# Optimization experiments

Hardware: AMD Instinct MI355X
Metric: run time of the kernel (lower is better)

## Reference

```python
import jax, jax.numpy as jnp
import numpy as np

VOCAB = 32000
D_MODEL = 768
N_LAYERS = 2
D_STATE = 16
D_CONV = 4
EXPAND = 2
D_INNER = EXPAND * D_MODEL            # 1536
DT_RANK = (D_MODEL + 15) // 16        # 48
B, L = 2, 1024


def setup_inputs() -> dict:
    key = jax.random.key(0)
    ks = jax.random.split(key, 10)
    n = lambda k, shape, s=0.02: jax.random.normal(k, shape, jnp.float32) * s
    A_log = jnp.broadcast_to(
        jnp.log(jnp.arange(1, D_STATE + 1, dtype=jnp.float32)),
        (N_LAYERS, D_INNER, D_STATE)).copy()
    return {
        "x": jax.random.randint(ks[0], (B, L), 0, VOCAB, jnp.int32),
        "embedding": n(ks[1], (VOCAB, D_MODEL)),
        "in_proj_w": n(ks[2], (N_LAYERS, 2 * D_INNER, D_MODEL)),
        "conv_w": n(ks[3], (N_LAYERS, D_INNER, D_CONV), 0.1),
        "conv_b": jnp.zeros((N_LAYERS, D_INNER), jnp.float32),
        "x_proj_w": n(ks[4], (N_LAYERS, DT_RANK + 2 * D_STATE, D_INNER)),
        "dt_proj_w": n(ks[5], (N_LAYERS, D_INNER, DT_RANK), 0.1),
        "dt_proj_b": jnp.full((N_LAYERS, D_INNER), -4.6, jnp.float32),  # softplus(-4.6)~0.01
        "A_log": A_log,
        "D_param": jnp.ones((N_LAYERS, D_INNER), jnp.float32),
        "out_proj_w": n(ks[6], (N_LAYERS, D_MODEL, D_INNER)),
        "ln_w": jnp.ones((D_MODEL,), jnp.float32),
        "ln_b": jnp.zeros((D_MODEL,), jnp.float32),
    }


def _causal_conv1d(x, w, b):
    # x: (B,L,Din), w: (Din,K) depthwise, b: (Din,)  -> (B,L,Din), causal
    Din, K = w.shape
    xt = jnp.transpose(x, (0, 2, 1))  # (B,Din,L)
    out = jax.lax.conv_general_dilated(
        xt, w[:, None, :], window_strides=(1,), padding=[(K - 1, 0)],
        feature_group_count=Din)
    return jnp.transpose(out, (0, 2, 1)) + b


def _selective_scan(u, dt, A, Bm, Cm, Dp):
    # u,dt: (B,L,Din); A: (Din,N); Bm,Cm: (B,L,N); Dp: (Din,)
    dA = jnp.exp(jnp.einsum('bld,dn->bldn', dt, A))          # (B,L,Din,N)
    dBu = jnp.einsum('bld,bln,bld->bldn', dt, Bm, u)          # (B,L,Din,N)

    def step(h, inp):
        dA_t, dBu_t, C_t = inp
        h = dA_t * h + dBu_t                                   # (B,Din,N)
        y = jnp.einsum('bdn,bn->bd', h, C_t)
        return h, y

    h0 = jnp.zeros((u.shape[0], u.shape[2], A.shape[1]), u.dtype)
    _, ys = jax.lax.scan(step, h0, (dA.transpose(1, 0, 2, 3),
                                    dBu.transpose(1, 0, 2, 3),
                                    Cm.transpose(1, 0, 2)))
    return ys.transpose(1, 0, 2) + u * Dp                      # (B,L,Din)


def _mamba_block(h, in_w, cw, cb, xp_w, dt_w, dt_b, A_log, Dp, out_w):
    xz = jnp.einsum('bld,ed->ble', h, in_w)                    # (B,L,2*Din)
    x_in, z = jnp.split(xz, 2, axis=-1)
    xc = jax.nn.silu(_causal_conv1d(x_in, cw, cb))             # (B,L,Din)
    x_dbl = jnp.einsum('bld,ed->ble', xc, xp_w)                # (B,L,dt_rank+2N)
    dt, Bm, Cm = jnp.split(x_dbl, [DT_RANK, DT_RANK + D_STATE], axis=-1)
    dt = jax.nn.softplus(jnp.einsum('blr,dr->bld', dt, dt_w) + dt_b)
    A = -jnp.exp(A_log)                                        # (Din,N)
    y = _selective_scan(xc, dt, A, Bm, Cm, Dp)
    y = y * jax.nn.silu(z)
    return jnp.einsum('bld,ed->ble', y, out_w)                 # (B,L,d_model)


def _layer_norm(x, w, b, eps=1e-5):
    mu = x.mean(-1, keepdims=True)
    var = ((x - mu) ** 2).mean(-1, keepdims=True)
    return (x - mu) * jax.lax.rsqrt(var + eps) * w + b


def reference(x, embedding, in_proj_w, conv_w, conv_b, x_proj_w, dt_proj_w,
              dt_proj_b, A_log, D_param, out_proj_w, ln_w, ln_b):
    h = embedding[x]                                           # (B,L,d_model)
    for i in range(N_LAYERS):
        h = _mamba_block(h, in_proj_w[i], conv_w[i], conv_b[i], x_proj_w[i],
                         dt_proj_w[i], dt_proj_b[i], A_log[i], D_param[i],
                         out_proj_w[i]) + h
    h = _layer_norm(h, ln_w, ln_b)
    return jnp.einsum('bld,vd->blv', h, embedding)             # tied lm_head
```

## Files before the change

kernel.cpp:

```cpp
#include <hip/hip_runtime.h>
#include <hip/hip_bf16.h>

typedef __bf16 bf16_t;
typedef __bf16 bf16x8 __attribute__((ext_vector_type(8)));
typedef float floatx4 __attribute__((ext_vector_type(4)));

#define D_MODEL 768
#define D_INNER 1536
#define D_STATE 16
#define DT_RANK 48
#define NROWS 2048
#define LSEQ 1024
#define SCAN_C 32
#define SCAN_RPC 32
#define SCAN_NDG 24
#define SCAN_STRIDE 24576

__global__ void detect_kernel(const unsigned int* __restrict__ lnw, int* __restrict__ flag) {
  if (threadIdx.x == 0 && blockIdx.x == 0)
    *flag = (lnw[0] == 0x3F800000u) ? 0 : 1;
}

struct CvtSrcs { const void* p[11]; };

__global__ __launch_bounds__(256) void cvt_all(CvtSrcs sp, bf16_t* __restrict__ wk,
                                               int total, const int* __restrict__ flagp) {
  int i = blockIdx.x * 256 + threadIdx.x;
  if (i >= total) return;
  const int off[12] = {0, 4718592, 4730880, 4733952, 4979712, 5127168, 5130240,
                       5179392, 5182464, 7541760, 7542528, 7543296};
  const void* src = sp.p[0];
  int base = 0;
#pragma unroll
  for (int k = 1; k <= 10; k++) {
    if (i >= off[k]) { src = sp.p[k]; base = off[k]; }
  }
  int j = i - base;
  float v = (*flagp) ? (float)((const bf16_t*)src)[j] : ((const float*)src)[j];
  wk[i] = (bf16_t)v;
}

__global__ __launch_bounds__(256) void cvt_emb(const void* __restrict__ src,
                                               bf16_t* __restrict__ dst,
                                               const int* __restrict__ flagp) {
  int i = blockIdx.x * 256 + threadIdx.x;
  const int nchunk = 32000 * 768 / 8;
  if (i >= nchunk) return;
  if (*flagp) {
    ((uint4*)dst)[i] = ((const uint4*)src)[i];
  } else {
    const float4* s = (const float4*)src + (size_t)i * 2;
    float4 f0 = s[0], f1 = s[1];
    bf16x8 v;
    v[0] = (bf16_t)f0.x; v[1] = (bf16_t)f0.y; v[2] = (bf16_t)f0.z; v[3] = (bf16_t)f0.w;
    v[4] = (bf16_t)f1.x; v[5] = (bf16_t)f1.y; v[6] = (bf16_t)f1.z; v[7] = (bf16_t)f1.w;
    *(bf16x8*)(dst + (size_t)i * 8) = v;
  }
}

__global__ __launch_bounds__(256) void embed_kernel(const int* __restrict__ x,
                                                    const void* __restrict__ emb,
                                                    float* __restrict__ h,
                                                    bf16_t* __restrict__ hb,
                                                    const int* __restrict__ flagp) {
  int isbf = *flagp;
  int idx = blockIdx.x * 256 + threadIdx.x;
  if (idx >= NROWS * D_MODEL) return;
  int row = idx / D_MODEL, c = idx - row * D_MODEL;
  size_t o = (size_t)x[row] * D_MODEL + c;
  float v = isbf ? (float)((const bf16_t*)emb)[o] : ((const float*)emb)[o];
  h[idx] = v;
  hb[idx] = (bf16_t)v;
}

typedef __attribute__((address_space(3))) void lds_void_t;
typedef __attribute__((address_space(1))) void glb_void_t;

__device__ __forceinline__ void gload16(const void* g, void* l) {
  __builtin_amdgcn_global_load_lds((const glb_void_t*)(unsigned long long)g,
                                   (lds_void_t*)(unsigned long long)l, 16, 0, 0);
}

__global__ __launch_bounds__(256) void gemm_bt(const bf16_t* __restrict__ A,
                                               const void* __restrict__ Bw,
                                               int M, int N, int K, int mode,
                                               float* __restrict__ Cf,
                                               bf16_t* __restrict__ Cb,
                                               const float* __restrict__ res,
                                               const int* __restrict__ flagp,
                                               int swapgrid) {
  __shared__ __align__(16) bf16_t As[128 * 64];
  __shared__ __align__(16) bf16_t Bs[128 * 64];
  int bNative = flagp ? (*flagp == 0) : 0;
  int tid = threadIdx.x;
  int nb = swapgrid ? blockIdx.y : blockIdx.x;
  int mb = swapgrid ? blockIdx.x : blockIdx.y;
  int m0 = mb * 128, n0 = nb * 128;
  int wave = tid >> 6, lane = tid & 63;
  int wr = wave >> 1, wc = wave & 1;
  int m16 = lane & 15, ksel = lane >> 4;
  int srow = lane >> 3;
  int sseg = lane & 7;

  floatx4 acc[4][4];
#pragma unroll
  for (int i = 0; i < 4; i++)
#pragma unroll
    for (int j = 0; j < 4; j++) acc[i][j] = (floatx4){0.f, 0.f, 0.f, 0.f};

  for (int k0 = 0; k0 < K; k0 += 64) {
#pragma unroll
    for (int i = 0; i < 4; i++) {
      int j = wave * 4 + i;
      int row = j * 8 + srow;
      int sg = sseg ^ (row & 7);
      gload16(A + (size_t)(m0 + row) * K + k0 + sg * 8, &As[j * 512]);
    }
    if (!bNative) {
#pragma unroll
      for (int i = 0; i < 4; i++) {
        int j = wave * 4 + i;
        int row = j * 8 + srow;
        int sg = sseg ^ (row & 7);
        gload16((const bf16_t*)Bw + (size_t)(n0 + row) * K + k0 + sg * 8, &Bs[j * 512]);
      }
    } else {
#pragma unroll
      for (int rep = 0; rep < 4; rep++) {
        int l = tid + rep * 256;
        int row = l >> 3, sg = l & 7;
        const float* gb = (const float*)Bw + (size_t)(n0 + row) * K + k0 + sg * 8;
        float4 f0 = *(const float4*)gb;
        float4 f1 = *(const float4*)(gb + 4);
        bf16x8 v;
        v[0] = (bf16_t)f0.x; v[1] = (bf16_t)f0.y; v[2] = (bf16_t)f0.z; v[3] = (bf16_t)f0.w;
        v[4] = (bf16_t)f1.x; v[5] = (bf16_t)f1.y; v[6] = (bf16_t)f1.z; v[7] = (bf16_t)f1.w;
        *(bf16x8*)&Bs[row * 64 + (sg ^ (row & 7)) * 8] = v;
      }
    }
    __syncthreads();
#pragma unroll
    for (int kk = 0; kk < 2; kk++) {
      int ck = (ksel + 4 * kk) ^ (lane & 7);
      bf16x8 aF[4], bF[4];
#pragma unroll
      for (int mi = 0; mi < 4; mi++)
        aF[mi] = *(const bf16x8*)&As[(wr * 64 + mi * 16 + m16) * 64 + ck * 8];
#pragma unroll
      for (int ni = 0; ni < 4; ni++)
        bF[ni] = *(const bf16x8*)&Bs[(wc * 64 + ni * 16 + m16) * 64 + ck * 8];
#pragma unroll
      for (int mi = 0; mi < 4; mi++)
#pragma unroll
        for (int ni = 0; ni < 4; ni++)
          acc[mi][ni] = __builtin_amdgcn_mfma_f32_16x16x32_bf16(aF[mi], bF[ni], acc[mi][ni], 0, 0, 0);
    }
    __syncthreads();
  }

#pragma unroll
  for (int mi = 0; mi < 4; mi++)
#pragma unroll
    for (int ni = 0; ni < 4; ni++)
#pragma unroll
      for (int r = 0; r < 4; r++) {
        int row = m0 + wr * 64 + mi * 16 + ksel * 4 + r;
        int col = n0 + wc * 64 + ni * 16 + m16;
        size_t off = (size_t)row * N + col;
        float v = acc[mi][ni][r];
        if (mode == 0) {
          Cf[off] = v;
        } else if (mode == 1) {
          float o = v + res[off];
          Cf[off] = o;
          Cb[off] = (bf16_t)o;
        } else {
          Cf[off] = v;
        }
      }
}

__global__ __launch_bounds__(256) void conv_silu(const float* __restrict__ xz,
                                                 const bf16_t* __restrict__ cw,
                                                 const bf16_t* __restrict__ cb,
                                                 bf16_t* __restrict__ xc) {
  int idx = blockIdx.x * 256 + threadIdx.x;
  if (idx >= NROWS * D_INNER) return;
  int d = idx % D_INNER;
  int row = idx / D_INNER;
  int l = row % LSEQ;
  int base = row - l;
  float s = (float)cb[d];
#pragma unroll
  for (int k = 0; k < 4; k++) {
    int ll = l - 3 + k;
    if (ll >= 0) s += (float)cw[d * 4 + k] * xz[(size_t)(base + ll) * (2 * D_INNER) + d];
  }
  float sil = s / (1.f + __expf(-s));
  xc[idx] = (bf16_t)sil;
}

__device__ inline float bflo(unsigned int u) { return __uint_as_float(u << 16); }
__device__ inline float bfhi(unsigned int u) { return __uint_as_float(u & 0xffff0000u); }

__global__ __launch_bounds__(128) void xproj_kernel(const bf16_t* __restrict__ xc,
                                                    const bf16_t* __restrict__ W,
                                                    float* __restrict__ xdbl) {
  __shared__ unsigned int srow[D_INNER / 2];
  int row = blockIdx.x;
  const unsigned int* src = (const unsigned int*)(xc + (size_t)row * D_INNER);
  for (int i = threadIdx.x; i < D_INNER / 2; i += 128) srow[i] = src[i];
  __syncthreads();
  int j = threadIdx.x;
  if (j < DT_RANK + 2 * D_STATE) {
    const unsigned int* wr = (const unsigned int*)(W + (size_t)j * D_INNER);
    float s = 0.f;
    for (int i = 0; i < D_INNER / 2; i++) {
      unsigned int a = srow[i], w = wr[i];
      s = fmaf(bflo(a), bflo(w), s);
      s = fmaf(bfhi(a), bfhi(w), s);
    }
    xdbl[(size_t)row * 80 + j] = s;
  }
}

__global__ __launch_bounds__(256) void dtproj_kernel(const float* __restrict__ xdbl,
                                                     const bf16_t* __restrict__ W,
                                                     const bf16_t* __restrict__ bias,
                                                     float* __restrict__ dt) {
  int idx = blockIdx.x * 256 + threadIdx.x;
  if (idx >= NROWS * D_INNER) return;
  int d = idx % D_INNER;
  int row = idx / D_INNER;
  const bf16_t* wr = W + (size_t)d * DT_RANK;
  const float* xr = xdbl + (size_t)row * 80;
  float s = (float)bias[d];
#pragma unroll 8
  for (int r = 0; r < DT_RANK; r++) s = fmaf(xr[r], (float)wr[r], s);
  float sp = (s > 20.f) ? s : log1pf(__expf(s));
  dt[idx] = sp;
}

__global__ __launch_bounds__(64) void scan_p1(const float* __restrict__ dt_,
                                              const bf16_t* __restrict__ xc,
                                              const float* __restrict__ xdbl,
                                              const bf16_t* __restrict__ A_log,
                                              float* __restrict__ P,
                                              float* __restrict__ F) {
  int wg = blockIdx.x;
  int dgrp = wg % SCAN_NDG, c2 = wg / SCAN_NDG;
  int b = c2 >> 5, c = c2 & 31;
  int d = dgrp * 64 + threadIdx.x;
  int r0 = b * LSEQ + c * SCAN_RPC;

  float Adn[16];
  {
    bf16x8 a0 = *(const bf16x8*)(A_log + (size_t)d * 16);
    bf16x8 a1 = *(const bf16x8*)(A_log + (size_t)d * 16 + 8);
#pragma unroll
    for (int n = 0; n < 8; n++) { Adn[n] = -__expf((float)a0[n]); Adn[n + 8] = -__expf((float)a1[n]); }
  }
  float h[16], p[16];
#pragma unroll
  for (int n = 0; n < 16; n++) { h[n] = 0.f; p[n] = 1.f; }

  float dtv = dt_[(size_t)r0 * D_INNER + d];
  float uv = (float)xc[(size_t)r0 * D_INNER + d];
  float Bv[16];
  {
    const float4* bp = (const float4*)(xdbl + (size_t)r0 * 80 + DT_RANK);
#pragma unroll
    for (int q = 0; q < 4; q++) *(float4*)&Bv[q * 4] = bp[q];
  }

  for (int i = 0; i < SCAN_RPC; i++) {
    int rn = r0 + i + 1;
    float dtn = dt_[(size_t)rn * D_INNER + d];
    float un = (float)xc[(size_t)rn * D_INNER + d];
    float Bn[16];
    {
      const float4* bp = (const float4*)(xdbl + (size_t)rn * 80 + DT_RANK);
#pragma unroll
      for (int q = 0; q < 4; q++) *(float4*)&Bn[q * 4] = bp[q];
    }
    float dtu = dtv * uv;
#pragma unroll
    for (int n = 0; n < 16; n++) {
      float dA = __expf(dtv * Adn[n]);
      h[n] = fmaf(dA, h[n], dtu * Bv[n]);
      p[n] *= dA;
    }
    dtv = dtn; uv = un;
#pragma unroll
    for (int n = 0; n < 16; n++) Bv[n] = Bn[n];
  }

  size_t o = (size_t)c2 * SCAN_STRIDE + (size_t)d * 16;
#pragma unroll
  for (int q = 0; q < 4; q++) {
    *(float4*)(P + o + q * 4) = *(float4*)&p[q * 4];
    *(float4*)(F + o + q * 4) = *(float4*)&h[q * 4];
  }
}

__global__ __launch_bounds__(256) void scan_p2(const float* __restrict__ P,
                                               const float* __restrict__ F,
                                               float* __restrict__ Hin) {
  int gid = blockIdx.x * 256 + threadIdx.x;
  if (gid >= 2 * SCAN_STRIDE) return;
  int b = gid / SCAN_STRIDE, j = gid - b * SCAN_STRIDE;
  float pP[SCAN_C], pF[SCAN_C];
#pragma unroll
  for (int c = 0; c < SCAN_C; c++) {
    size_t o = (size_t)(b * SCAN_C + c) * SCAN_STRIDE + j;
    pP[c] = P[o]; pF[c] = F[o];
  }
  float h = 0.f;
#pragma unroll
  for (int c = 0; c < SCAN_C; c++) {
    size_t o = (size_t)(b * SCAN_C + c) * SCAN_STRIDE + j;
    Hin[o] = h;
    h = fmaf(pP[c], h, pF[c]);
  }
}

__global__ __launch_bounds__(64) void scan_p3(const float* __restrict__ dt_,
                                              const bf16_t* __restrict__ xc,
                                              const float* __restrict__ xdbl,
                                              const float* __restrict__ xz,
                                              const bf16_t* __restrict__ A_log,
                                              const bf16_t* __restrict__ Dp,
                                              const float* __restrict__ Hin,
                                              bf16_t* __restrict__ yg) {
  int wg = blockIdx.x;
  int dgrp = wg % SCAN_NDG, c2 = wg / SCAN_NDG;
  int b = c2 >> 5, c = c2 & 31;
  int d = dgrp * 64 + threadIdx.x;
  int r0 = b * LSEQ + c * SCAN_RPC;

  float Adn[16];
  {
    bf16x8 a0 = *(const bf16x8*)(A_log + (size_t)d * 16);
    bf16x8 a1 = *(const bf16x8*)(A_log + (size_t)d * 16 + 8);
#pragma unroll
    for (int n = 0; n < 8; n++) { Adn[n] = -__expf((float)a0[n]); Adn[n + 8] = -__expf((float)a1[n]); }
  }
  float Dd = (float)Dp[d];
  float h[16];
  {
    size_t o = (size_t)c2 * SCAN_STRIDE + (size_t)d * 16;
#pragma unroll
    for (int q = 0; q < 4; q++) *(float4*)&h[q * 4] = *(const float4*)(Hin + o + q * 4);
  }

  float dtv = dt_[(size_t)r0 * D_INNER + d];
  float uv = (float)xc[(size_t)r0 * D_INNER + d];
  float zv = xz[(size_t)r0 * (2 * D_INNER) + D_INNER + d];
  float Bv[16], Cv[16];
  {
    const float4* bp = (const float4*)(xdbl + (size_t)r0 * 80 + DT_RANK);
#pragma unroll
    for (int q = 0; q < 4; q++) *(float4*)&Bv[q * 4] = bp[q];
#pragma unroll
    for (int q = 0; q < 4; q++) *(float4*)&Cv[q * 4] = bp[q + 4];
  }

  for (int i = 0; i < SCAN_RPC; i++) {
    int r = r0 + i;
    int rn = r + 1;
    float dtn = dt_[(size_t)rn * D_INNER + d];
    float un = (float)xc[(size_t)rn * D_INNER + d];
    float zn = xz[(size_t)rn * (2 * D_INNER) + D_INNER + d];
    float Bn[16], Cn[16];
    {
      const float4* bp = (const float4*)(xdbl + (size_t)rn * 80 + DT_RANK);
#pragma unroll
      for (int q = 0; q < 4; q++) *(float4*)&Bn[q * 4] = bp[q];
#pragma unroll
      for (int q = 0; q < 4; q++) *(float4*)&Cn[q * 4] = bp[q + 4];
    }
    float dtu = dtv * uv;
    float y = 0.f;
#pragma unroll
    for (int n = 0; n < 16; n++) {
      float dA = __expf(dtv * Adn[n]);
      h[n] = fmaf(dA, h[n], dtu * Bv[n]);
      y = fmaf(h[n], Cv[n], y);
    }
    float sil = zv / (1.f + __expf(-zv));
    yg[(size_t)r * D_INNER + d] = (bf16_t)((y + Dd * uv) * sil);
    dtv = dtn; uv = un; zv = zn;
#pragma unroll
    for (int n = 0; n < 16; n++) { Bv[n] = Bn[n]; Cv[n] = Cn[n]; }
  }
}

__global__ __launch_bounds__(256) void ln_kernel(const float* __restrict__ h,
                                                 const bf16_t* __restrict__ w,
                                                 const bf16_t* __restrict__ b,
                                                 bf16_t* __restrict__ out) {
  __shared__ float s1[4], s2[4];
  int row = blockIdx.x;
  int tid = threadIdx.x, lane = tid & 63, wave = tid >> 6;
  const float* hr = h + (size_t)row * D_MODEL;
  float a = 0.f, a2 = 0.f;
  for (int i = tid; i < D_MODEL; i += 256) {
    float v = hr[i];
    a += v; a2 += v * v;
  }
#pragma unroll
  for (int m = 32; m >= 1; m >>= 1) {
    a += __shfl_xor(a, m, 64);
    a2 += __shfl_xor(a2, m, 64);
  }
  if (lane == 0) { s1[wave] = a; s2[wave] = a2; }
  __syncthreads();
  float sum = s1[0] + s1[1] + s1[2] + s1[3];
  float sum2 = s2[0] + s2[1] + s2[2] + s2[3];
  float mu = sum / D_MODEL;
  float var = sum2 / D_MODEL - mu * mu;
  float inv = rsqrtf(var + 1e-5f);
  for (int i = tid; i < D_MODEL; i += 256)
    out[(size_t)row * D_MODEL + i] = (bf16_t)((hr[i] - mu) * inv * (float)w[i] + (float)b[i]);
}

extern "C" void kernel_launch(void* const* d_in, const int* in_sizes, int n_in,
                              void* d_out, int out_size, void* d_ws, size_t ws_size,
                              hipStream_t stream) {
  const int* x = (const int*)d_in[0];
  const void* emb = d_in[1];
  float* out = (float*)d_out;

  char* ob = (char*)d_out;
  float* h = (float*)(ob + 0);
  bf16_t* hb = (bf16_t*)(ob + 6291456);
  float* xz = (float*)(ob + 9437184);
  bf16_t* xc = (bf16_t*)(ob + 34603008);
  float* xdbl = (float*)(ob + 40894464);
  float* dt = (float*)(ob + 41549824);
  bf16_t* yg = (bf16_t*)(ob + 54132736);
  bf16_t* wk = (bf16_t*)(ob + 60424192);
  float* scanP = (float*)(ob + 75510784);
  float* scanF = (float*)(ob + 81802240);
  float* scanH = (float*)(ob + 88093696);
  bf16_t* lno = (bf16_t*)d_ws;
  int* flag = (int*)((char*)d_ws + 3145728);
  bf16_t* embb = (bf16_t*)((char*)d_ws + 3145744);
  bool bigws = ws_size >= (size_t)3145744 + 49152000u;

  bf16_t* c_inw  = wk + 0;
  bf16_t* c_cw   = wk + 4718592;
  bf16_t* c_cb   = wk + 4730880;
  bf16_t* c_xpw  = wk + 4733952;
  bf16_t* c_dtw  = wk + 4979712;
  bf16_t* c_dtb  = wk + 5127168;
  bf16_t* c_alog = wk + 5130240;
  bf16_t* c_dp   = wk + 5179392;
  bf16_t* c_outw = wk + 5182464;
  bf16_t* c_lnw  = wk + 7541760;
  bf16_t* c_lnb  = wk + 7542528;

  detect_kernel<<<1, 64, 0, stream>>>((const unsigned int*)d_in[11], flag);

  CvtSrcs srcs;
  for (int k = 0; k < 11; k++) srcs.p[k] = d_in[k + 2];
  const int cvt_total = 7543296;
  cvt_all<<<(cvt_total + 255) / 256, 256, 0, stream>>>(srcs, wk, cvt_total, flag);

  if (bigws)
    cvt_emb<<<(32000 * 768 / 8 + 255) / 256, 256, 0, stream>>>(emb, embb, flag);

  embed_kernel<<<(NROWS * D_MODEL + 255) / 256, 256, 0, stream>>>(x, emb, h, hb, flag);

  for (int i = 0; i < 2; i++) {
    gemm_bt<<<dim3(3072 / 128, NROWS / 128), 256, 0, stream>>>(
        hb, c_inw + (size_t)i * 2 * D_INNER * D_MODEL, NROWS, 2 * D_INNER, D_MODEL,
        0, xz, nullptr, nullptr, nullptr, 0);
    conv_silu<<<(NROWS * D_INNER + 255) / 256, 256, 0, stream>>>(
        xz, c_cw + (size_t)i * D_INNER * 4, c_cb + (size_t)i * D_INNER, xc);
    xproj_kernel<<<NROWS, 128, 0, stream>>>(xc, c_xpw + (size_t)i * 80 * D_INNER, xdbl);
    dtproj_kernel<<<(NROWS * D_INNER + 255) / 256, 256, 0, stream>>>(
        xdbl, c_dtw + (size_t)i * D_INNER * DT_RANK, c_dtb + (size_t)i * D_INNER, dt);
    scan_p1<<<2 * SCAN_C * SCAN_NDG, 64, 0, stream>>>(
        dt, xc, xdbl, c_alog + (size_t)i * D_INNER * D_STATE, scanP, scanF);
    scan_p2<<<(2 * SCAN_STRIDE + 255) / 256, 256, 0, stream>>>(scanP, scanF, scanH);
    scan_p3<<<2 * SCAN_C * SCAN_NDG, 64, 0, stream>>>(
        dt, xc, xdbl, xz, c_alog + (size_t)i * D_INNER * D_STATE,
        c_dp + (size_t)i * D_INNER, scanH, yg);
    gemm_bt<<<dim3(D_MODEL / 128, NROWS / 128), 256, 0, stream>>>(
        yg, c_outw + (size_t)i * D_MODEL * D_INNER, NROWS, D_MODEL, D_INNER,
        1, h, hb, h, nullptr, 0);
  }

  ln_kernel<<<NROWS, 256, 0, stream>>>(h, c_lnw, c_lnb, lno);

  if (bigws)
    gemm_bt<<<dim3(NROWS / 128, 32000 / 128), 256, 0, stream>>>(
        lno, embb, NROWS, 32000, D_MODEL, 2, out, nullptr, nullptr, nullptr, 1);
  else
    gemm_bt<<<dim3(NROWS / 128, 32000 / 128), 256, 0, stream>>>(
        lno, emb, NROWS, 32000, D_MODEL, 2, out, nullptr, nullptr, flag, 1);
}
```

Measured before the change: 1.008 ms.

## Run x_proj on the MFMA GEMM, remap GEMM workgroups per XCD, vectorize dt_proj

The scalar per-row x_proj kernel is replaced by the tiled MFMA GEMM. Its weight is zero-padded from 80 to 128 rows and a new epilogue mode writes only the first 80 columns. GEMM launches gain a swizzled block mapping that groups workgroups by (lin & 7), so blocks sharing B tiles land on the same XCD for better L2 reuse. dt_proj now uses vectorized bf16x8/float4 loads. The cost is 48 wasted padded columns, and x_proj launches only 16 workgroups.

```diff
diff --git a/kernel.cpp b/kernel.cpp
--- a/kernel.cpp
+++ b/kernel.cpp
@@ -38,6 +38,16 @@
   int j = i - base;
   float v = (*flagp) ? (float)((const bf16_t*)src)[j] : ((const float*)src)[j];
   wk[i] = (bf16_t)v;
+}
+
+__global__ __launch_bounds__(256) void pad_xpw(const bf16_t* __restrict__ src,
+                                               bf16_t* __restrict__ dst) {
+  int i = blockIdx.x * 256 + threadIdx.x;
+  if (i >= 2 * 128 * 1536) return;
+  int c = i % 1536;
+  int r = (i / 1536) % 128;
+  int lay = i / (128 * 1536);
+  dst[i] = (r < 80) ? src[((size_t)lay * 80 + r) * 1536 + c] : (bf16_t)0.f;
 }
 
 __global__ __launch_bounds__(256) void cvt_emb(const void* __restrict__ src,
@@ -93,8 +103,19 @@
   __shared__ __align__(16) bf16_t Bs[128 * 64];
   int bNative = flagp ? (*flagp == 0) : 0;
   int tid = threadIdx.x;
-  int nb = swapgrid ? blockIdx.y : blockIdx.x;
-  int mb = swapgrid ? blockIdx.x : blockIdx.y;
+  int mb, nb;
+  if (swapgrid == 2) {
+    int nwg = gridDim.x * gridDim.y;
+    int lin = blockIdx.y * gridDim.x + blockIdx.x;
+    int cpx = nwg >> 3;
+    int nid = (lin & 7) * cpx + (lin >> 3);
+    mb = nid & 15;
+    nb = nid >> 4;
+  } else if (swapgrid == 1) {
+    mb = blockIdx.x; nb = blockIdx.y;
+  } else {
+    nb = blockIdx.x; mb = blockIdx.y;
+  }
   int m0 = mb * 128, n0 = nb * 128;
   int wave = tid >> 6, lane = tid & 63;
   int wr = wave >> 1, wc = wave & 1;
@@ -174,8 +195,10 @@
           float o = v + res[off];
           Cf[off] = o;
           Cb[off] = (bf16_t)o;
+        } else if (mode == 2) {
+          Cf[off] = v;
         } else {
-          Cf[off] = v;
+          if (col < 80) Cf[(size_t)row * 80 + col] = v;
         }
       }
 }
@@ -200,30 +223,6 @@
   xc[idx] = (bf16_t)sil;
 }
 
-__device__ inline float bflo(unsigned int u) { return __uint_as_float(u << 16); }
-__device__ inline float bfhi(unsigned int u) { return __uint_as_float(u & 0xffff0000u); }
-
-__global__ __launch_bounds__(128) void xproj_kernel(const bf16_t* __restrict__ xc,
-                                                    const bf16_t* __restrict__ W,
-                                                    float* __restrict__ xdbl) {
-  __shared__ unsigned int srow[D_INNER / 2];
-  int row = blockIdx.x;
-  const unsigned int* src = (const unsigned int*)(xc + (size_t)row * D_INNER);
-  for (int i = threadIdx.x; i < D_INNER / 2; i += 128) srow[i] = src[i];
-  __syncthreads();
-  int j = threadIdx.x;
-  if (j < DT_RANK + 2 * D_STATE) {
-    const unsigned int* wr = (const unsigned int*)(W + (size_t)j * D_INNER);
-    float s = 0.f;
-    for (int i = 0; i < D_INNER / 2; i++) {
-      unsigned int a = srow[i], w = wr[i];
-      s = fmaf(bflo(a), bflo(w), s);
-      s = fmaf(bfhi(a), bfhi(w), s);
-    }
-    xdbl[(size_t)row * 80 + j] = s;
-  }
-}
-
 __global__ __launch_bounds__(256) void dtproj_kernel(const float* __restrict__ xdbl,
                                                      const bf16_t* __restrict__ W,
                                                      const bf16_t* __restrict__ bias,
@@ -232,11 +231,18 @@
   if (idx >= NROWS * D_INNER) return;
   int d = idx % D_INNER;
   int row = idx / D_INNER;
-  const bf16_t* wr = W + (size_t)d * DT_RANK;
-  const float* xr = xdbl + (size_t)row * 80;
+  const bf16x8* w8 = (const bf16x8*)(W + (size_t)d * DT_RANK);
+  const float4* x4 = (const float4*)(xdbl + (size_t)row * 80);
   float s = (float)bias[d];
-#pragma unroll 8
-  for (int r = 0; r < DT_RANK; r++) s = fmaf(xr[r], (float)wr[r], s);
+#pragma unroll
+  for (int q = 0; q < 6; q++) {
+    bf16x8 w = w8[q];
+    float4 a = x4[q * 2], b = x4[q * 2 + 1];
+    s = fmaf(a.x, (float)w[0], s); s = fmaf(a.y, (float)w[1], s);
+    s = fmaf(a.z, (float)w[2], s); s = fmaf(a.w, (float)w[3], s);
+    s = fmaf(b.x, (float)w[4], s); s = fmaf(b.y, (float)w[5], s);
+    s = fmaf(b.z, (float)w[6], s); s = fmaf(b.w, (float)w[7], s);
+  }
   float sp = (s > 20.f) ? s : log1pf(__expf(s));
   dt[idx] = sp;
 }
@@ -440,9 +446,10 @@
   float* dt = (float*)(ob + 41549824);
   bf16_t* yg = (bf16_t*)(ob + 54132736);
   bf16_t* wk = (bf16_t*)(ob + 60424192);
-  float* scanP = (float*)(ob + 75510784);
-  float* scanF = (float*)(ob + 81802240);
-  float* scanH = (float*)(ob + 88093696);
+  bf16_t* c_xpwp = (bf16_t*)(ob + 75510784);
+  float* scanP = (float*)(ob + 76297216);
+  float* scanF = (float*)(ob + 82588672);
+  float* scanH = (float*)(ob + 88880128);
   bf16_t* lno = (bf16_t*)d_ws;
   int* flag = (int*)((char*)d_ws + 3145728);
   bf16_t* embb = (bf16_t*)((char*)d_ws + 3145744);
@@ -466,6 +473,7 @@
   for (int k = 0; k < 11; k++) srcs.p[k] = d_in[k + 2];
   const int cvt_total = 7543296;
   cvt_all<<<(cvt_total + 255) / 256, 256, 0, stream>>>(srcs, wk, cvt_total, flag);
+  pad_xpw<<<(2 * 128 * 1536 + 255) / 256, 256, 0, stream>>>(c_xpw, c_xpwp);
 
   if (bigws)
     cvt_emb<<<(32000 * 768 / 8 + 255) / 256, 256, 0, stream>>>(emb, embb, flag);
@@ -473,12 +481,14 @@
   embed_kernel<<<(NROWS * D_MODEL + 255) / 256, 256, 0, stream>>>(x, emb, h, hb, flag);
 
   for (int i = 0; i < 2; i++) {
-    gemm_bt<<<dim3(3072 / 128, NROWS / 128), 256, 0, stream>>>(
+    gemm_bt<<<dim3(16, 3072 / 128), 256, 0, stream>>>(
         hb, c_inw + (size_t)i * 2 * D_INNER * D_MODEL, NROWS, 2 * D_INNER, D_MODEL,
-        0, xz, nullptr, nullptr, nullptr, 0);
+        0, xz, nullptr, nullptr, nullptr, 2);
     conv_silu<<<(NROWS * D_INNER + 255) / 256, 256, 0, stream>>>(
         xz, c_cw + (size_t)i * D_INNER * 4, c_cb + (size_t)i * D_INNER, xc);
-    xproj_kernel<<<NROWS, 128, 0, stream>>>(xc, c_xpw + (size_t)i * 80 * D_INNER, xdbl);
+    gemm_bt<<<dim3(1, NROWS / 128), 256, 0, stream>>>(
+        xc, c_xpwp + (size_t)i * 128 * D_INNER, NROWS, 128, D_INNER,
+        3, xdbl, nullptr, nullptr, nullptr, 0);
     dtproj_kernel<<<(NROWS * D_INNER + 255) / 256, 256, 0, stream>>>(
         xdbl, c_dtw + (size_t)i * D_INNER * DT_RANK, c_dtb + (size_t)i * D_INNER, dt);
     scan_p1<<<2 * SCAN_C * SCAN_NDG, 64, 0, stream>>>(
@@ -487,17 +497,17 @@
     scan_p3<<<2 * SCAN_C * SCAN_NDG, 64, 0, stream>>>(
         dt, xc, xdbl, xz, c_alog + (size_t)i * D_INNER * D_STATE,
         c_dp + (size_t)i * D_INNER, scanH, yg);
-    gemm_bt<<<dim3(D_MODEL / 128, NROWS / 128), 256, 0, stream>>>(
+    gemm_bt<<<dim3(16, D_MODEL / 128), 256, 0, stream>>>(
         yg, c_outw + (size_t)i * D_MODEL * D_INNER, NROWS, D_MODEL, D_INNER,
-        1, h, hb, h, nullptr, 0);
+        1, h, hb, h, nullptr, 2);
   }
 
   ln_kernel<<<NROWS, 256, 0, stream>>>(h, c_lnw, c_lnb, lno);
 
   if (bigws)
-    gemm_bt<<<dim3(NROWS / 128, 32000 / 128), 256, 0, stream>>>(
-        lno, embb, NROWS, 32000, D_MODEL, 2, out, nullptr, nullptr, nullptr, 1);
+    gemm_bt<<<dim3(16, 32000 / 128), 256, 0, stream>>>(
+        lno, embb, NROWS, 32000, D_MODEL, 2, out, nullptr, nullptr, nullptr, 2);
   else
-    gemm_bt<<<dim3(NROWS / 128, 32000 / 128), 256, 0, stream>>>(
-        lno, emb, NROWS, 32000, D_MODEL, 2, out, nullptr, nullptr, flag, 1);
-}
+    gemm_bt<<<dim3(16, 32000 / 128), 256, 0, stream>>>(
+        lno, emb, NROWS, 32000, D_MODEL, 2, out, nullptr, nullptr, flag, 2);
+}
```

Measured after the change: 948.0 us. 1.06x faster.
